# Performance work log

Hardware: AMD Instinct MI355X
Metric: run time of the kernel (lower is better)

Reference implementation:

```python
import jax, jax.numpy as jnp
import numpy as np

D = 2048          # hidden_size
H = 16            # num attention heads
HD = D // H       # head_dim = 128
DFF = 8192        # intermediate_size
DLCA = 4096       # d_lca = 2*hidden_size
EPS = 1e-6
LAM, TAU, DT, NSTEPS = 0.1, 0.1, 0.01, 10
ROPE_THETA = 10000.0


def rmsnorm(x, w):
    v = jnp.mean(x.astype(jnp.float32) ** 2, axis=-1, keepdims=True)
    return (x * jax.lax.rsqrt(v + EPS)).astype(x.dtype) * w


def rope_cos_sin(seq_len, dtype):
    inv_freq = 1.0 / (ROPE_THETA ** (jnp.arange(0, HD, 2, dtype=jnp.float32) / HD))
    t = jnp.arange(seq_len, dtype=jnp.float32)
    freqs = jnp.outer(t, inv_freq)              # [S, HD/2]
    emb = jnp.concatenate([freqs, freqs], -1)   # [S, HD]
    return jnp.cos(emb).astype(dtype), jnp.sin(emb).astype(dtype)


def rotate_half(x):
    x1, x2 = jnp.split(x, 2, axis=-1)
    return jnp.concatenate([-x2, x1], axis=-1)


def setup_inputs() -> dict:
    key = jax.random.key(0)
    ks = jax.random.split(key, 10)
    s = 0.02
    return {
        "hidden_states": jax.random.normal(ks[0], (2, 2048, D), jnp.float32),
        "w_ln_in": jnp.ones((D,), jnp.float32),
        "w_ln_lca": jnp.ones((D,), jnp.float32),
        "w_ln_post": jnp.ones((D,), jnp.float32),
        "Wq": jax.random.normal(ks[1], (D, D), jnp.float32) * s,
        "Wk": jax.random.normal(ks[2], (D, D), jnp.float32) * s,
        "Wv": jax.random.normal(ks[3], (D, D), jnp.float32) * s,
        "Wo": jax.random.normal(ks[4], (D, D), jnp.float32) * s,
        "W_lca": jax.random.normal(ks[5], (D, DLCA), jnp.float32) * s,
        "W_gate": jax.random.normal(ks[6], (D, DFF), jnp.float32) * s,
        "W_up": jax.random.normal(ks[7], (D, DFF), jnp.float32) * s,
        "W_down": jax.random.normal(ks[8], (DFF, D), jnp.float32) * s,
    }


def reference(hidden_states, w_ln_in, w_ln_lca, w_ln_post, Wq, Wk, Wv, Wo,
              W_lca, W_gate, W_up, W_down):
    B, S, _ = hidden_states.shape
    residual = hidden_states

    # --- causal self-attention with RoPE ---
    h = rmsnorm(hidden_states, w_ln_in)
    q = (h @ Wq).reshape(B, S, H, HD).transpose(0, 2, 1, 3)  # [B,H,S,HD]
    k = (h @ Wk).reshape(B, S, H, HD).transpose(0, 2, 1, 3)
    v = (h @ Wv).reshape(B, S, H, HD).transpose(0, 2, 1, 3)
    cos, sin = rope_cos_sin(S, h.dtype)
    q = q * cos + rotate_half(q) * sin
    k = k * cos + rotate_half(k) * sin
    scores = jnp.einsum('bhqd,bhkd->bhqk', q, k) / jnp.sqrt(jnp.asarray(HD, h.dtype))
    causal = jnp.tril(jnp.ones((S, S), bool))
    scores = jnp.where(causal, scores, jnp.finfo(scores.dtype).min)
    probs = jax.nn.softmax(scores, axis=-1)
    attn = jnp.einsum('bhqk,bhkd->bhqd', probs, v)
    attn = attn.transpose(0, 2, 1, 3).reshape(B, S, D) @ Wo
    h = residual + attn

    # --- LCA: project up, 10-step lateral-competition recurrence, project back ---
    hn = rmsnorm(h, w_ln_lca)
    xf = hn.reshape(-1, D)                       # [B*S, D]
    b = xf @ W_lca                               # [B*S, DLCA]
    G = W_lca.T @ W_lca                          # [DLCA, DLCA]
    G = G - jnp.diag(jnp.diag(G))                # zero diagonal (self-inhibition)
    u = jnp.zeros_like(b)
    for _ in range(NSTEPS):
        a = jax.nn.relu(u - LAM)
        u = u + DT * ((b - a @ G - u) / TAU)
    a = jax.nn.relu(u - LAM)
    h = (a @ W_lca.T).reshape(B, S, D)           # LCA REPLACES the residual stream

    # --- MLP (SwiGLU) with residual ---
    residual = h
    m = rmsnorm(h, w_ln_post)
    mlp = (jax.nn.silu(m @ W_gate) * (m @ W_up)) @ W_down
    return residual + mlp
```

## Files before the change

kernel.cpp:

```cpp
#include <hip/hip_runtime.h>
#include <hip/hip_fp8.h>

typedef short bf16x8 __attribute__((ext_vector_type(8)));
typedef float f32x4 __attribute__((ext_vector_type(4)));
typedef long long ll;

__device__ __forceinline__ unsigned short f2bf(float f) {
    union { float f; unsigned u; } v; v.f = f;
    unsigned u = v.u;
    unsigned r = (u + 0x7FFFu + ((u >> 16) & 1u)) >> 16;
    return (unsigned short)r;
}
__device__ __forceinline__ float bf2f(unsigned short h) {
    union { unsigned u; float f; } v; v.u = ((unsigned)h) << 16; return v.f;
}
__device__ __forceinline__ unsigned char f2fp8(float f) {
    __hip_fp8_e4m3 q(f);
    return (unsigned char)q.__x;
}

typedef const __attribute__((address_space(1))) void gas_void;
typedef __attribute__((address_space(3))) void las_void;
__device__ __forceinline__ void gll16(const void* g, void* l) {
    __builtin_amdgcn_global_load_lds((gas_void*)g, (las_void*)l, 16, 0, 0);
}

__global__ __launch_bounds__(256) void gemm_bf16(
    const unsigned short* __restrict__ A, ll lda, ll sAz,
    const unsigned short* __restrict__ B, ll ldb, ll sBz,
    void* __restrict__ C, ll ldc, ll sCz,
    int M, int N, int K,
    float alpha, int mode, int causal,
    const float* __restrict__ res)
{
    __shared__ unsigned short sA[2][4096];
    __shared__ unsigned short sB[2][4096];
    const int n0 = blockIdx.x * 128;
    const int m0 = blockIdx.y * 128;
    if (causal && n0 > m0) return;
    const int z = blockIdx.z;

    const unsigned short* Ab = A + (ll)z * sAz + (ll)m0 * lda;
    const unsigned short* Bb = B + (ll)z * sBz + (ll)n0 * ldb;

    const int t    = threadIdx.x;
    const int lane = t & 63;
    const int w    = t >> 6, wm = w >> 1, wn = w & 1;
    const int m16  = lane & 15, quad = lane >> 4;

    const int r0 = t >> 2, cs = t & 3;
    const int r1 = r0 + 64;
    const int c0 = cs ^ ((r0 >> 1) & 3);
    const int c1 = cs ^ ((r1 >> 1) & 3);
    const ll a_off0 = (ll)r0 * lda + c0 * 8;
    const ll a_off1 = (ll)r1 * lda + c1 * 8;
    const ll b_off0 = (ll)r0 * ldb + c0 * 8;
    const ll b_off1 = (ll)r1 * ldb + c1 * 8;
    const int dst = t * 8;

    int aoff[4], boff[4];
#pragma unroll
    for (int mi = 0; mi < 4; mi++) {
        int rr = wm * 64 + mi * 16 + m16;
        aoff[mi] = rr * 32 + ((quad ^ ((rr >> 1) & 3)) << 3);
    }
#pragma unroll
    for (int ni = 0; ni < 4; ni++) {
        int rr = wn * 64 + ni * 16 + m16;
        boff[ni] = rr * 32 + ((quad ^ ((rr >> 1) & 3)) << 3);
    }

    f32x4 acc[4][4];
#pragma unroll
    for (int i = 0; i < 4; i++)
#pragma unroll
        for (int j = 0; j < 4; j++) acc[i][j] = (f32x4){0.f, 0.f, 0.f, 0.f};

    gll16(Ab + a_off0, sA[0] + dst);
    gll16(Ab + a_off1, sA[0] + 2048 + dst);
    gll16(Bb + b_off0, sB[0] + dst);
    gll16(Bb + b_off1, sB[0] + 2048 + dst);
    __syncthreads();

    for (int kt = 0; kt < K; kt += 32) {
        const int cur = (kt >> 5) & 1;
        if (kt + 32 < K) {
            const int nxt = cur ^ 1;
            gll16(Ab + a_off0 + kt + 32, sA[nxt] + dst);
            gll16(Ab + a_off1 + kt + 32, sA[nxt] + 2048 + dst);
            gll16(Bb + b_off0 + kt + 32, sB[nxt] + dst);
            gll16(Bb + b_off1 + kt + 32, sB[nxt] + 2048 + dst);
        }
        bf16x8 af[4], bg[4];
#pragma unroll
        for (int mi = 0; mi < 4; mi++) af[mi] = *(const bf16x8*)(sA[cur] + aoff[mi]);
#pragma unroll
        for (int ni = 0; ni < 4; ni++) bg[ni] = *(const bf16x8*)(sB[cur] + boff[ni]);
#pragma unroll
        for (int mi = 0; mi < 4; mi++)
#pragma unroll
            for (int ni = 0; ni < 4; ni++)
                acc[mi][ni] = __builtin_amdgcn_mfma_f32_16x16x32_bf16(
                    af[mi], bg[ni], acc[mi][ni], 0, 0, 0);
        __syncthreads();
    }

    const ll czoff = (ll)z * sCz;
#pragma unroll
    for (int mi = 0; mi < 4; mi++) {
#pragma unroll
        for (int ni = 0; ni < 4; ni++) {
#pragma unroll
            for (int r = 0; r < 4; r++) {
                int row = m0 + wm * 64 + mi * 16 + quad * 4 + r;
                int col = n0 + wn * 64 + ni * 16 + m16;
                ll idx = czoff + (ll)row * ldc + col;
                float v = acc[mi][ni][r] * alpha;
                if (mode == 0) {
                    ((float*)C)[idx] = res ? (v + res[idx]) : v;
                } else if (mode == 1) {
                    ((unsigned short*)C)[idx] = f2bf(v);
                } else {
                    ((unsigned char*)C)[idx] = (row == col) ? (unsigned char)0 : f2fp8(v);
                }
            }
        }
    }
}

__global__ __launch_bounds__(256) void gemm_fp8(
    const unsigned char* __restrict__ A, ll lda,
    const unsigned char* __restrict__ B, ll ldb,
    int M, int N, int K, float alpha, int mode,
    unsigned short* __restrict__ uu, const unsigned short* __restrict__ cc,
    void* __restrict__ Out)
{
    __shared__ unsigned char sA[2][8192];
    __shared__ unsigned char sB[2][8192];
    const int n0 = blockIdx.x * 128;
    const int m0 = blockIdx.y * 128;

    const unsigned char* Ab = A + (ll)m0 * lda;
    const unsigned char* Bb = B + (ll)n0 * ldb;

    const int t    = threadIdx.x;
    const int lane = t & 63;
    const int w    = t >> 6, wm = w >> 1, wn = w & 1;
    const int m16  = lane & 15, quad = lane >> 4;

    const int r0 = t >> 2, cs = t & 3;
    const int r1 = r0 + 64;
    const int c0 = cs ^ ((r0 >> 1) & 3);
    const int c1 = cs ^ ((r1 >> 1) & 3);
    const ll a_off0 = (ll)r0 * lda + c0 * 16;
    const ll a_off1 = (ll)r1 * lda + c1 * 16;
    const ll b_off0 = (ll)r0 * ldb + c0 * 16;
    const ll b_off1 = (ll)r1 * ldb + c1 * 16;
    const int dst = t * 16;

    int aoff[4][2], boff[4][2];
#pragma unroll
    for (int mi = 0; mi < 4; mi++) {
        int rr = wm * 64 + mi * 16 + m16;
#pragma unroll
        for (int kh = 0; kh < 2; kh++) {
            int ch = kh * 2 + (quad >> 1);
            aoff[mi][kh] = rr * 64 + ((ch ^ ((rr >> 1) & 3)) << 4) + ((quad & 1) << 3);
        }
    }
#pragma unroll
    for (int ni = 0; ni < 4; ni++) {
        int rr = wn * 64 + ni * 16 + m16;
#pragma unroll
        for (int kh = 0; kh < 2; kh++) {
            int ch = kh * 2 + (quad >> 1);
            boff[ni][kh] = rr * 64 + ((ch ^ ((rr >> 1) & 3)) << 4) + ((quad & 1) << 3);
        }
    }

    f32x4 acc[4][4];
#pragma unroll
    for (int i = 0; i < 4; i++)
#pragma unroll
        for (int j = 0; j < 4; j++) acc[i][j] = (f32x4){0.f, 0.f, 0.f, 0.f};

    gll16(Ab + a_off0, sA[0] + dst);
    gll16(Ab + a_off1, sA[0] + 4096 + dst);
    gll16(Bb + b_off0, sB[0] + dst);
    gll16(Bb + b_off1, sB[0] + 4096 + dst);
    __syncthreads();

    for (int kt = 0; kt < K; kt += 64) {
        const int cur = (kt >> 6) & 1;
        if (kt + 64 < K) {
            const int nxt = cur ^ 1;
            gll16(Ab + a_off0 + kt + 64, sA[nxt] + dst);
            gll16(Ab + a_off1 + kt + 64, sA[nxt] + 4096 + dst);
            gll16(Bb + b_off0 + kt + 64, sB[nxt] + dst);
            gll16(Bb + b_off1 + kt + 64, sB[nxt] + 4096 + dst);
        }
#pragma unroll
        for (int kh = 0; kh < 2; kh++) {
            long long af[4], bg[4];
#pragma unroll
            for (int mi = 0; mi < 4; mi++)
                af[mi] = *(const long long*)(sA[cur] + aoff[mi][kh]);
#pragma unroll
            for (int ni = 0; ni < 4; ni++)
                bg[ni] = *(const long long*)(sB[cur] + boff[ni][kh]);
#pragma unroll
            for (int mi = 0; mi < 4; mi++)
#pragma unroll
                for (int ni = 0; ni < 4; ni++)
                    acc[mi][ni] = __builtin_amdgcn_mfma_f32_16x16x32_fp8_fp8(
                        af[mi], bg[ni], acc[mi][ni], 0, 0, 0);
        }
        __syncthreads();
    }

#pragma unroll
    for (int mi = 0; mi < 4; mi++) {
#pragma unroll
        for (int ni = 0; ni < 4; ni++) {
#pragma unroll
            for (int r = 0; r < 4; r++) {
                int row = m0 + wm * 64 + mi * 16 + quad * 4 + r;
                int col = n0 + wn * 64 + ni * 16 + m16;
                ll idx = (ll)row * N + col;
                float v = acc[mi][ni][r] * alpha;
                float un = 0.9f * bf2f(uu[idx]) + bf2f(cc[idx]) - v;
                uu[idx] = f2bf(un);
                float a = fmaxf(un - 0.1f, 0.0f);
                if (mode == 3) ((unsigned char*)Out)[idx] = f2fp8(a * 8.0f);
                else           ((unsigned short*)Out)[idx] = f2bf(a);
            }
        }
    }
}


__global__ void wtrans_k(const float* __restrict__ in, unsigned short* __restrict__ out,
                         int R, int C) {
    __shared__ float tile[32][33];
    ll bx = (ll)blockIdx.x * 32, by = (ll)blockIdx.y * 32;
    int tx = threadIdx.x & 31, ty = threadIdx.x >> 5;
#pragma unroll
    for (int i = ty; i < 32; i += 8) tile[i][tx] = in[(by + i) * C + bx + tx];
    __syncthreads();
#pragma unroll
    for (int i = ty; i < 32; i += 8) out[(bx + i) * R + by + tx] = f2bf(tile[tx][i]);
}

__global__ void conv4_k(const float* __restrict__ in, unsigned short* __restrict__ out, ll n) {
    ll i = ((ll)blockIdx.x * 256 + threadIdx.x) * 4;
    if (i >= n) return;
    float4 v = *(const float4*)(in + i);
    out[i] = f2bf(v.x); out[i + 1] = f2bf(v.y); out[i + 2] = f2bf(v.z); out[i + 3] = f2bf(v.w);
}

__global__ void rmsnorm_k(const float* __restrict__ in, const float* __restrict__ w,
                          unsigned short* __restrict__ out) {
    int row = blockIdx.x, t = threadIdx.x;
    const float* x = in + (ll)row * 2048;
    float v[8]; float s = 0.f;
#pragma unroll
    for (int i = 0; i < 8; i++) { v[i] = x[t + i * 256]; s += v[i] * v[i]; }
#pragma unroll
    for (int o = 32; o > 0; o >>= 1) s += __shfl_xor(s, o, 64);
    __shared__ float rs[4];
    if ((t & 63) == 0) rs[t >> 6] = s;
    __syncthreads();
    s = (rs[0] + rs[1] + rs[2] + rs[3]) * (1.0f / 2048.0f);
    float sc = rsqrtf(s + 1e-6f);
    unsigned short* o_ = out + (ll)row * 2048;
#pragma unroll
    for (int i = 0; i < 8; i++) o_[t + i * 256] = f2bf(v[i] * sc * w[t + i * 256]);
}

__global__ void rope_k(unsigned short* __restrict__ q, unsigned short* __restrict__ k) {
    int idx = blockIdx.x * 256 + threadIdx.x;
    int j = idx & 63;
    int h = (idx >> 6) & 15;
    int row = idx >> 10;
    int s = row & 2047;
    float f = __expf(-(float)j * 0.14391156831212783f);
    float ang = (float)s * f;
    float sn, cs;
    sincosf(ang, &sn, &cs);
    ll base = (ll)row * 2048 + h * 128 + j;
    float x1 = bf2f(q[base]), x2 = bf2f(q[base + 64]);
    q[base]      = f2bf(x1 * cs - x2 * sn);
    q[base + 64] = f2bf(x2 * cs + x1 * sn);
    x1 = bf2f(k[base]); x2 = bf2f(k[base + 64]);
    k[base]      = f2bf(x1 * cs - x2 * sn);
    k[base + 64] = f2bf(x2 * cs + x1 * sn);
}

__global__ void vtrans_k(const unsigned short* __restrict__ in, unsigned short* __restrict__ out) {
    __shared__ unsigned short tile[32][33];
    int z = blockIdx.z, b = z >> 4, h = z & 15;
    const unsigned short* ib = in + (ll)b * 4194304 + h * 128;
    unsigned short* ob = out + (ll)z * 262144;
    int bx = blockIdx.x * 32, by = blockIdx.y * 32;
    int tx = threadIdx.x & 31, ty = threadIdx.x >> 5;
#pragma unroll
    for (int i = ty; i < 32; i += 8) tile[i][tx] = ib[(ll)(by + i) * 2048 + bx + tx];
    __syncthreads();
#pragma unroll
    for (int i = ty; i < 32; i += 8) ob[(ll)(bx + i) * 2048 + by + tx] = tile[tx][i];
}

__global__ void softmax_k(unsigned short* __restrict__ sc) {
    int q = blockIdx.x, z = blockIdx.y, t = threadIdx.x;
    unsigned short* row = sc + (ll)z * 4194304 + (ll)q * 2048;
    float x[8]; float m = -1e30f;
#pragma unroll
    for (int i = 0; i < 8; i++) {
        int kk = t + i * 256;
        x[i] = (kk <= q) ? bf2f(row[kk]) : -1e30f;
        m = fmaxf(m, x[i]);
    }
#pragma unroll
    for (int o = 32; o > 0; o >>= 1) m = fmaxf(m, __shfl_xor(m, o, 64));
    __shared__ float rm[4];
    if ((t & 63) == 0) rm[t >> 6] = m;
    __syncthreads();
    m = fmaxf(fmaxf(rm[0], rm[1]), fmaxf(rm[2], rm[3]));
    float s = 0.f;
#pragma unroll
    for (int i = 0; i < 8; i++) {
        int kk = t + i * 256;
        float e = (kk <= q) ? __expf(x[i] - m) : 0.0f;
        x[i] = e; s += e;
    }
#pragma unroll
    for (int o = 32; o > 0; o >>= 1) s += __shfl_xor(s, o, 64);
    __shared__ float rsum[4];
    if ((t & 63) == 0) rsum[t >> 6] = s;
    __syncthreads();
    s = rsum[0] + rsum[1] + rsum[2] + rsum[3];
    float inv = 1.0f / s;
#pragma unroll
    for (int i = 0; i < 8; i++) row[t + i * 256] = f2bf(x[i] * inv);
}

__global__ void lca_init_k(const unsigned short* __restrict__ c, unsigned short* __restrict__ u,
                           unsigned char* __restrict__ a) {
    ll i = ((ll)blockIdx.x * 256 + threadIdx.x) * 4;
#pragma unroll
    for (int j = 0; j < 4; j++) {
        unsigned short cv = c[i + j];
        u[i + j] = cv;
        a[i + j] = f2fp8(fmaxf(bf2f(cv) - 0.1f, 0.f) * 8.0f);
    }
}

__global__ void swiglu_k(unsigned short* __restrict__ g, const unsigned short* __restrict__ u) {
    ll i = ((ll)blockIdx.x * 256 + threadIdx.x) * 4;
#pragma unroll
    for (int j = 0; j < 4; j++) {
        float x = bf2f(g[i + j]);
        float y = bf2f(u[i + j]);
        float sil = x / (1.0f + __expf(-x));
        g[i + j] = f2bf(sil * y);
    }
}

extern "C" void kernel_launch(void* const* d_in, const int* in_sizes, int n_in,
                              void* d_out, int out_size, void* d_ws, size_t ws_size,
                              hipStream_t stream) {
    (void)in_sizes; (void)n_in; (void)out_size; (void)ws_size;
    const float* X        = (const float*)d_in[0];
    const float* wln_in   = (const float*)d_in[1];
    const float* wln_lca  = (const float*)d_in[2];
    const float* wln_post = (const float*)d_in[3];
    const float* Wq   = (const float*)d_in[4];
    const float* Wk   = (const float*)d_in[5];
    const float* Wv   = (const float*)d_in[6];
    const float* Wo   = (const float*)d_in[7];
    const float* Wlca = (const float*)d_in[8];
    const float* Wg   = (const float*)d_in[9];
    const float* Wu   = (const float*)d_in[10];
    const float* Wd   = (const float*)d_in[11];
    float* out = (float*)d_out;

    char* ws = (char*)d_ws;
    unsigned short* WqT = (unsigned short*)(ws);
    unsigned short* WkT = WqT + 4194304;
    unsigned short* WvT = WqT + 2 * 4194304;
    unsigned short* WoT = WqT + 3 * 4194304;
    unsigned short* WgT = WqT;
    unsigned short* WlcaT = (unsigned short*)(ws + 33554432);
    unsigned short* Wlcab = WlcaT + 8388608;
    unsigned short* WuT   = WlcaT;
    unsigned short* h_bf = (unsigned short*)(ws + 67108864);
    char* pool = ws + 83886080;
    unsigned short* qb     = (unsigned short*)(pool);
    unsigned short* kb     = (unsigned short*)(pool + 16777216);
    unsigned short* vb     = (unsigned short*)(pool + 33554432);
    unsigned short* VT     = (unsigned short*)(pool + 50331648);
    unsigned short* attn   = (unsigned short*)(pool + 67108864);
    unsigned short* scores = (unsigned short*)(pool + 83886080);
    float* h1              = (float*)(pool + 150994944);
    unsigned short* cbuf   = (unsigned short*)(pool);
    unsigned short* ubuf   = (unsigned short*)(pool + 33554432);
    unsigned char* a8_0    = (unsigned char*)(pool + 67108864);
    unsigned char* a8_1    = (unsigned char*)(pool + 83886080);
    unsigned short* abf    = (unsigned short*)(pool + 100663296);
    unsigned char* Gf8     = (unsigned char*)(pool + 134217728);
    float* h2              = (float*)(pool + 150994944);
    unsigned short* gate   = (unsigned short*)(pool);
    unsigned short* up     = (unsigned short*)(pool + 67108864);
    unsigned short* WdT    = (unsigned short*)(pool + 201326592);

    dim3 blk(256);
    auto gemm = [&](const unsigned short* A, ll lda, ll sAz,
                    const unsigned short* Bt, ll ldb, ll sBz,
                    void* C, ll ldc, ll sCz,
                    int M, int N, int K, int Z,
                    float alpha, int mode, int causal, const float* res) {
        dim3 g(N / 128, M / 128, Z);
        gemm_bf16<<<g, blk, 0, stream>>>(A, lda, sAz, Bt, ldb, sBz, C, ldc, sCz,
                                         M, N, K, alpha, mode, causal, res);
    };

    wtrans_k<<<dim3(64, 64), blk, 0, stream>>>(Wq, WqT, 2048, 2048);
    wtrans_k<<<dim3(64, 64), blk, 0, stream>>>(Wk, WkT, 2048, 2048);
    wtrans_k<<<dim3(64, 64), blk, 0, stream>>>(Wv, WvT, 2048, 2048);
    wtrans_k<<<dim3(64, 64), blk, 0, stream>>>(Wo, WoT, 2048, 2048);
    wtrans_k<<<dim3(128, 64), blk, 0, stream>>>(Wlca, WlcaT, 2048, 4096);
    conv4_k<<<8192, blk, 0, stream>>>(Wlca, Wlcab, 8388608LL);

    rmsnorm_k<<<4096, blk, 0, stream>>>(X, wln_in, h_bf);
    gemm(h_bf, 2048, 0, WqT, 2048, 0, qb, 2048, 0, 4096, 2048, 2048, 1, 1.f, 1, 0, nullptr);
    gemm(h_bf, 2048, 0, WkT, 2048, 0, kb, 2048, 0, 4096, 2048, 2048, 1, 1.f, 1, 0, nullptr);
    gemm(h_bf, 2048, 0, WvT, 2048, 0, vb, 2048, 0, 4096, 2048, 2048, 1, 1.f, 1, 0, nullptr);
    rope_k<<<16384, blk, 0, stream>>>(qb, kb);
    vtrans_k<<<dim3(4, 64, 32), blk, 0, stream>>>(vb, VT);
    for (int c = 0; c < 4; c++) {
        int b = c >> 1, h0 = (c & 1) * 8;
        const unsigned short* qbase = qb + (ll)b * 4194304 + h0 * 128;
        const unsigned short* kbase = kb + (ll)b * 4194304 + h0 * 128;
        gemm(qbase, 2048, 128, kbase, 2048, 128, scores, 2048, 4194304LL,
             2048, 2048, 128, 8, 0.08838834764831845f, 1, 1, nullptr);
        softmax_k<<<dim3(2048, 8), blk, 0, stream>>>(scores);
        const unsigned short* vtb = VT + (ll)(b * 16 + h0) * 262144;
        unsigned short* ab = attn + (ll)b * 4194304 + h0 * 128;
        gemm(scores, 2048, 4194304LL, vtb, 2048, 262144LL, ab, 2048, 128,
             2048, 128, 2048, 8, 1.f, 1, 0, nullptr);
    }
    gemm(attn, 2048, 0, WoT, 2048, 0, h1, 2048, 0, 4096, 2048, 2048, 1, 1.f, 0, 0, X);

    rmsnorm_k<<<4096, blk, 0, stream>>>(h1, wln_lca, h_bf);
    gemm(WlcaT, 2048, 0, WlcaT, 2048, 0, Gf8, 4096, 0, 4096, 4096, 2048, 1, 16.f, 2, 0, nullptr);
    gemm(h_bf, 2048, 0, WlcaT, 2048, 0, cbuf, 4096, 0, 4096, 4096, 2048, 1, 0.1f, 1, 0, nullptr);
    lca_init_k<<<16384, blk, 0, stream>>>(cbuf, ubuf, a8_0);
    unsigned char* acur = a8_0; unsigned char* anext = a8_1;
    for (int i = 0; i < 9; i++) {
        int mode = (i < 8) ? 3 : 4;
        void* outp = (i < 8) ? (void*)anext : (void*)abf;
        gemm_fp8<<<dim3(32, 32), blk, 0, stream>>>(
            acur, 4096, Gf8, 4096, 4096, 4096, 4096,
            0.1f / 128.0f, mode, ubuf, cbuf, outp);
        unsigned char* tmp = acur; acur = anext; anext = tmp;
    }
    gemm(abf, 4096, 0, Wlcab, 4096, 0, h2, 2048, 0, 4096, 2048, 4096, 1, 1.f, 0, 0, nullptr);

    wtrans_k<<<dim3(256, 64), blk, 0, stream>>>(Wg, WgT, 2048, 8192);
    wtrans_k<<<dim3(256, 64), blk, 0, stream>>>(Wu, WuT, 2048, 8192);
    wtrans_k<<<dim3(64, 256), blk, 0, stream>>>(Wd, WdT, 8192, 2048);
    rmsnorm_k<<<4096, blk, 0, stream>>>(h2, wln_post, h_bf);
    gemm(h_bf, 2048, 0, WgT, 2048, 0, gate, 8192, 0, 4096, 8192, 2048, 1, 1.f, 1, 0, nullptr);
    gemm(h_bf, 2048, 0, WuT, 2048, 0, up, 8192, 0, 4096, 8192, 2048, 1, 1.f, 1, 0, nullptr);
    swiglu_k<<<32768, blk, 0, stream>>>(gate, up);
    gemm(gate, 8192, 0, WdT, 8192, 0, out, 2048, 0, 4096, 2048, 8192, 1, 1.f, 0, 0, h2);
}
```

Measured before the change: 3.324 ms.

## Add 256-tile pipelined bf16/fp8 GEMMs and fuse QKV and gate/up projections

Adds new 512-thread GEMM kernels: a 256x256 bf16 kernel, a 128x256 bf16 kernel with a triple-buffered LDS ring, and a 256x256 fp8 kernel for the LCA recurrence. All use XCD-aware workgroup remapping, interleaved LDS prefetch, and MFMA priority bumps. The Q/K/V projections become one GEMM into a fused [4096,6144] buffer, and gate/up become one GEMM into [4096,16384], so rope, vtrans, attention and swiglu now index the interleaved layouts. The larger tiles increase operand reuse and cut launch count, at the cost of more registers and LDS per block and fewer blocks on the smaller GEMMs. The fused QKV GEMM reads its weights from WqT with ldb 2048 across 6144 output columns, which assumes WqT, WkT and WvT sit contiguously in the workspace.

```diff
diff --git a/kernel.cpp b/kernel.cpp
--- a/kernel.cpp
+++ b/kernel.cpp
@@ -23,6 +23,445 @@
 typedef __attribute__((address_space(3))) void las_void;
 __device__ __forceinline__ void gll16(const void* g, void* l) {
     __builtin_amdgcn_global_load_lds((gas_void*)g, (las_void*)l, 16, 0, 0);
+}
+
+#define BAR __builtin_amdgcn_s_barrier()
+#define LGKM0 do { asm volatile("s_waitcnt lgkmcnt(0)" ::: "memory"); __builtin_amdgcn_sched_barrier(0); } while (0)
+#define VMC(n) asm volatile("s_waitcnt vmcnt(" #n ")" ::: "memory")
+
+__global__ __launch_bounds__(512, 2) void gemm256_k(
+    const unsigned short* __restrict__ A, ll lda,
+    const unsigned short* __restrict__ B, ll ldb,
+    void* __restrict__ C, ll ldc,
+    int K, float alpha, int mode, const float* __restrict__ res)
+{
+    __shared__ unsigned short sA[2][2][8192];
+    __shared__ unsigned short sB[2][2][8192];
+
+    const int nwg = gridDim.x * gridDim.y;
+    int id = blockIdx.y * gridDim.x + blockIdx.x;
+    { int q = nwg >> 3, r = nwg & 7, x = id & 7, bb = id >> 3;
+      id = (x < r ? x * (q + 1) : r * (q + 1) + (x - r) * q) + bb; }
+    const int n0 = (id % gridDim.x) * 256;
+    const int m0 = (id / gridDim.x) * 256;
+
+    const unsigned short* Ab = A + (ll)m0 * lda;
+    const unsigned short* Bb = B + (ll)n0 * ldb;
+
+    const int t = threadIdx.x;
+    const int lane = t & 63;
+    const int w = t >> 6, wm = w >> 2, wn = w & 3;
+    const int m16 = lane & 15, quad = lane >> 4;
+
+    const int tr = t >> 3;
+    const int tc8 = ((t & 7) ^ (tr & 7)) << 3;
+
+    const int pk0 = m16 * 64 + (((quad    ) ^ (m16 & 7)) << 3);
+    const int pk1 = m16 * 64 + (((4 + quad) ^ (m16 & 7)) << 3);
+
+    auto stA = [&](int tile, int h) {
+        char* d0 = (char*)&sA[tile & 1][h][0] + t * 16;
+        const unsigned short* s0 = Ab + (ll)(h * 128 + tr) * lda + tc8 + (ll)tile * 64;
+        gll16(s0, d0);
+        gll16(s0 + 64 * lda, d0 + 8192);
+    };
+    auto stB = [&](int tile, int h) {
+        char* d0 = (char*)&sB[tile & 1][h][0] + t * 16;
+        const unsigned short* s0 = Bb + (ll)(h * 128 + tr) * ldb + tc8 + (ll)tile * 64;
+        gll16(s0, d0);
+        gll16(s0 + 64 * ldb, d0 + 8192);
+    };
+    auto ldA = [&](int s, int g, bf16x8 (&af)[4][2]) {
+        const unsigned short* p0 = &sA[s][wm][g * 4096];
+#pragma unroll
+        for (int a2 = 0; a2 < 4; a2++) {
+            af[a2][0] = *(const bf16x8*)(p0 + a2 * 1024 + pk0);
+            af[a2][1] = *(const bf16x8*)(p0 + a2 * 1024 + pk1);
+        }
+    };
+    auto ldB = [&](int s, int g, bf16x8 (&bg)[2][2]) {
+        const unsigned short* p0 = &sB[s][wn >> 1][(wn & 1) * 4096 + g * 2048];
+#pragma unroll
+        for (int b2 = 0; b2 < 2; b2++) {
+            bg[b2][0] = *(const bf16x8*)(p0 + b2 * 1024 + pk0);
+            bg[b2][1] = *(const bf16x8*)(p0 + b2 * 1024 + pk1);
+        }
+    };
+
+    f32x4 acc[8][4];
+#pragma unroll
+    for (int i = 0; i < 8; i++)
+#pragma unroll
+        for (int j = 0; j < 4; j++) acc[i][j] = (f32x4){0.f, 0.f, 0.f, 0.f};
+
+    bf16x8 afA[4][2], afB[4][2], bgA[2][2], bgB[2][2];
+
+#define MM256(af, bg, gm, gn) do { \
+    __builtin_amdgcn_s_setprio(1); \
+    _Pragma("unroll") \
+    for (int a2 = 0; a2 < 4; a2++) \
+    _Pragma("unroll") \
+    for (int b2 = 0; b2 < 2; b2++) { \
+        acc[(gm)*4+a2][(gn)*2+b2] = __builtin_amdgcn_mfma_f32_16x16x32_bf16(af[a2][0], bg[b2][0], acc[(gm)*4+a2][(gn)*2+b2], 0, 0, 0); \
+        acc[(gm)*4+a2][(gn)*2+b2] = __builtin_amdgcn_mfma_f32_16x16x32_bf16(af[a2][1], bg[b2][1], acc[(gm)*4+a2][(gn)*2+b2], 0, 0, 0); \
+    } \
+    __builtin_amdgcn_s_setprio(0); \
+} while (0)
+
+    stB(0, 0); stB(0, 1); stA(0, 0); stA(0, 1); stB(1, 0); stB(1, 1);
+    VMC(4); BAR;
+
+#define ITER256(T, LAST) do { \
+     \
+    stA((T) + 1, 0); \
+    ldA(0, 0, afA); ldB(0, 0, bgA); \
+    BAR; LGKM0; \
+    MM256(afA, bgA, 0, 0); \
+    BAR; \
+     \
+    stA((T) + 1, 1); \
+    ldB(0, 1, bgB); \
+    BAR; LGKM0; \
+    MM256(afA, bgB, 0, 1); \
+    BAR; \
+     \
+    if (!(LAST)) stB((T) + 2, 0); \
+    ldA(0, 1, afB); \
+    BAR; LGKM0; \
+    MM256(afB, bgA, 1, 0); \
+    BAR; \
+     \
+    if (!(LAST)) stB((T) + 2, 1); \
+    MM256(afB, bgB, 1, 1); \
+    if (LAST) { VMC(0); } else { VMC(4); } \
+    BAR; \
+     \
+    if (!(LAST)) stA((T) + 2, 0); \
+    ldA(1, 0, afA); ldB(1, 0, bgA); \
+    BAR; LGKM0; \
+    MM256(afA, bgA, 0, 0); \
+    BAR; \
+     \
+    if (!(LAST)) stA((T) + 2, 1); \
+    ldB(1, 1, bgB); \
+    BAR; LGKM0; \
+    MM256(afA, bgB, 0, 1); \
+    BAR; \
+     \
+    if (!(LAST)) stB((T) + 3, 0); \
+    ldA(1, 1, afB); \
+    BAR; LGKM0; \
+    MM256(afB, bgA, 1, 0); \
+    BAR; \
+     \
+    if (!(LAST)) stB((T) + 3, 1); \
+    MM256(afB, bgB, 1, 1); \
+    if (!(LAST)) { VMC(4); BAR; } \
+} while (0)
+
+    const int nIter = K >> 7;
+    for (int i = 0; i < nIter - 1; ++i) ITER256(2 * i, false);
+    ITER256(2 * (nIter - 1), true);
+
+#pragma unroll
+    for (int mi = 0; mi < 8; mi++) {
+#pragma unroll
+        for (int ni = 0; ni < 4; ni++) {
+#pragma unroll
+            for (int r4 = 0; r4 < 4; r4++) {
+                int row = m0 + wm * 128 + mi * 16 + quad * 4 + r4;
+                int col = n0 + wn * 64 + ni * 16 + m16;
+                ll idx = (ll)row * ldc + col;
+                float v = acc[mi][ni][r4] * alpha;
+                if (mode == 0) ((float*)C)[idx] = res ? (v + res[idx]) : v;
+                else if (mode == 1) ((unsigned short*)C)[idx] = f2bf(v);
+                else ((unsigned char*)C)[idx] = (row == col) ? (unsigned char)0 : f2fp8(v);
+            }
+        }
+    }
+}
+
+__global__ __launch_bounds__(512, 2) void gemm128_k(
+    const unsigned short* __restrict__ A, ll lda,
+    const unsigned short* __restrict__ B, ll ldb,
+    void* __restrict__ C, ll ldc,
+    int K, float alpha, int mode, const float* __restrict__ res)
+{
+    __shared__ unsigned short sA[3][8192];
+    __shared__ unsigned short sB[3][2][8192];
+
+    const int nwg = gridDim.x * gridDim.y;
+    int id = blockIdx.y * gridDim.x + blockIdx.x;
+    { int q = nwg >> 3, r = nwg & 7, x = id & 7, bb = id >> 3;
+      id = (x < r ? x * (q + 1) : r * (q + 1) + (x - r) * q) + bb; }
+    const int n0 = (id % gridDim.x) * 256;
+    const int m0 = (id / gridDim.x) * 128;
+
+    const unsigned short* Ab = A + (ll)m0 * lda;
+    const unsigned short* Bb = B + (ll)n0 * ldb;
+
+    const int t = threadIdx.x;
+    const int lane = t & 63;
+    const int w = t >> 6, wm = w >> 2, wn = w & 3;
+    const int m16 = lane & 15, quad = lane >> 4;
+
+    const int tr = t >> 3;
+    const int tc8 = ((t & 7) ^ (tr & 7)) << 3;
+    const int pk0 = m16 * 64 + (((quad    ) ^ (m16 & 7)) << 3);
+    const int pk1 = m16 * 64 + (((4 + quad) ^ (m16 & 7)) << 3);
+
+    auto stA = [&](int tile, int s) {
+        char* d0 = (char*)&sA[s][0] + t * 16;
+        const unsigned short* s0 = Ab + (ll)tr * lda + tc8 + (ll)tile * 64;
+        gll16(s0, d0);
+        gll16(s0 + 64 * lda, d0 + 8192);
+    };
+    auto stB2 = [&](int tile, int s) {
+#pragma unroll
+        for (int h = 0; h < 2; h++) {
+            char* d0 = (char*)&sB[s][h][0] + t * 16;
+            const unsigned short* s0 = Bb + (ll)(h * 128 + tr) * ldb + tc8 + (ll)tile * 64;
+            gll16(s0, d0);
+            gll16(s0 + 64 * ldb, d0 + 8192);
+        }
+    };
+    auto ldA4 = [&](int s, bf16x8 (&af)[4][2]) {
+        const unsigned short* p0 = &sA[s][wm * 4096];
+#pragma unroll
+        for (int a2 = 0; a2 < 4; a2++) {
+            af[a2][0] = *(const bf16x8*)(p0 + a2 * 1024 + pk0);
+            af[a2][1] = *(const bf16x8*)(p0 + a2 * 1024 + pk1);
+        }
+    };
+    auto ldB2 = [&](int s, int g, bf16x8 (&bg)[2][2]) {
+        const unsigned short* p0 = &sB[s][wn >> 1][(wn & 1) * 4096 + g * 2048];
+#pragma unroll
+        for (int b2 = 0; b2 < 2; b2++) {
+            bg[b2][0] = *(const bf16x8*)(p0 + b2 * 1024 + pk0);
+            bg[b2][1] = *(const bf16x8*)(p0 + b2 * 1024 + pk1);
+        }
+    };
+
+    f32x4 acc[4][4];
+#pragma unroll
+    for (int i = 0; i < 4; i++)
+#pragma unroll
+        for (int j = 0; j < 4; j++) acc[i][j] = (f32x4){0.f, 0.f, 0.f, 0.f};
+
+    bf16x8 af[4][2], bgA[2][2], bgB[2][2];
+
+#define MM128(bg, gn) do { \
+    __builtin_amdgcn_s_setprio(1); \
+    _Pragma("unroll") \
+    for (int a2 = 0; a2 < 4; a2++) \
+    _Pragma("unroll") \
+    for (int b2 = 0; b2 < 2; b2++) { \
+        acc[a2][(gn)*2+b2] = __builtin_amdgcn_mfma_f32_16x16x32_bf16(af[a2][0], bg[b2][0], acc[a2][(gn)*2+b2], 0, 0, 0); \
+        acc[a2][(gn)*2+b2] = __builtin_amdgcn_mfma_f32_16x16x32_bf16(af[a2][1], bg[b2][1], acc[a2][(gn)*2+b2], 0, 0, 0); \
+    } \
+    __builtin_amdgcn_s_setprio(0); \
+} while (0)
+
+    stA(0, 0); stB2(0, 0); stA(1, 1); stB2(1, 1);
+    VMC(6); BAR;
+
+    const int nT = K >> 6;
+    int sl = 0;
+    for (int T = 0; T < nT - 2; ++T) {
+        const int s2 = (sl >= 1) ? sl - 1 : 2;
+        stA(T + 2, s2);
+        ldA4(sl, af); ldB2(sl, 0, bgA);
+        BAR; LGKM0;
+        MM128(bgA, 0);
+        BAR;
+        stB2(T + 2, s2);
+        ldB2(sl, 1, bgB);
+        BAR; LGKM0;
+        MM128(bgB, 1);
+        VMC(6);
+        BAR;
+        sl = (sl >= 2) ? 0 : sl + 1;
+    }
+    {
+        ldA4(sl, af); ldB2(sl, 0, bgA);
+        BAR; LGKM0;
+        MM128(bgA, 0);
+        BAR;
+        ldB2(sl, 1, bgB);
+        BAR; LGKM0;
+        MM128(bgB, 1);
+        VMC(0);
+        BAR;
+        sl = (sl >= 2) ? 0 : sl + 1;
+    }
+    {
+        ldA4(sl, af); ldB2(sl, 0, bgA);
+        LGKM0;
+        MM128(bgA, 0);
+        ldB2(sl, 1, bgB);
+        LGKM0;
+        MM128(bgB, 1);
+    }
+
+#pragma unroll
+    for (int mi = 0; mi < 4; mi++) {
+#pragma unroll
+        for (int ni = 0; ni < 4; ni++) {
+#pragma unroll
+            for (int r4 = 0; r4 < 4; r4++) {
+                int row = m0 + wm * 64 + mi * 16 + quad * 4 + r4;
+                int col = n0 + wn * 64 + ni * 16 + m16;
+                ll idx = (ll)row * ldc + col;
+                float v = acc[mi][ni][r4] * alpha;
+                if (mode == 0) ((float*)C)[idx] = res ? (v + res[idx]) : v;
+                else if (mode == 1) ((unsigned short*)C)[idx] = f2bf(v);
+                else ((unsigned char*)C)[idx] = (row == col) ? (unsigned char)0 : f2fp8(v);
+            }
+        }
+    }
+}
+
+__global__ __launch_bounds__(512, 2) void gemm256f8_k(
+    const unsigned char* __restrict__ A, ll lda,
+    const unsigned char* __restrict__ B, ll ldb,
+    int N, int K, float alpha, int mode,
+    unsigned short* __restrict__ uu, const unsigned short* __restrict__ cc,
+    void* __restrict__ Out)
+{
+    __shared__ unsigned char sA[2][2][8192];
+    __shared__ unsigned char sB[2][2][8192];
+
+    const int nwg = gridDim.x * gridDim.y;
+    int id = blockIdx.y * gridDim.x + blockIdx.x;
+    { int q = nwg >> 3, r = nwg & 7, x = id & 7, bb = id >> 3;
+      id = (x < r ? x * (q + 1) : r * (q + 1) + (x - r) * q) + bb; }
+    const int n0 = (id % gridDim.x) * 256;
+    const int m0 = (id / gridDim.x) * 256;
+
+    const unsigned char* Ab = A + (ll)m0 * lda;
+    const unsigned char* Bb = B + (ll)n0 * ldb;
+
+    const int t = threadIdx.x;
+    const int lane = t & 63;
+    const int w = t >> 6, wm = w >> 2, wn = w & 3;
+    const int m16 = lane & 15, quad = lane >> 4;
+
+    const int tr8 = t >> 2;
+    const int tc16 = (((t & 3) ^ ((t >> 3) & 3)) << 4);
+
+    const int pq0 = m16 * 64 + ((((quad >> 1))     ^ ((m16 >> 1) & 3)) << 4) + ((quad & 1) << 3);
+    const int pq1 = m16 * 64 + (((2 + (quad >> 1)) ^ ((m16 >> 1) & 3)) << 4) + ((quad & 1) << 3);
+
+    auto stA = [&](int tile, int h) {
+        gll16(Ab + (ll)(h * 128 + tr8) * lda + tc16 + (ll)tile * 64,
+              (char*)&sA[tile & 1][h][0] + t * 16);
+    };
+    auto stB = [&](int tile, int h) {
+        gll16(Bb + (ll)(h * 128 + tr8) * ldb + tc16 + (ll)tile * 64,
+              (char*)&sB[tile & 1][h][0] + t * 16);
+    };
+    auto ldA8 = [&](int s, int g, ll (&af)[4][2]) {
+        const unsigned char* p0 = &sA[s][wm][g * 4096];
+#pragma unroll
+        for (int a2 = 0; a2 < 4; a2++) {
+            af[a2][0] = *(const ll*)(p0 + a2 * 1024 + pq0);
+            af[a2][1] = *(const ll*)(p0 + a2 * 1024 + pq1);
+        }
+    };
+    auto ldB8 = [&](int s, int g, ll (&bg)[2][2]) {
+        const unsigned char* p0 = &sB[s][wn >> 1][(wn & 1) * 4096 + g * 2048];
+#pragma unroll
+        for (int b2 = 0; b2 < 2; b2++) {
+            bg[b2][0] = *(const ll*)(p0 + b2 * 1024 + pq0);
+            bg[b2][1] = *(const ll*)(p0 + b2 * 1024 + pq1);
+        }
+    };
+
+    f32x4 acc[8][4];
+#pragma unroll
+    for (int i = 0; i < 8; i++)
+#pragma unroll
+        for (int j = 0; j < 4; j++) acc[i][j] = (f32x4){0.f, 0.f, 0.f, 0.f};
+
+    ll afA[4][2], afB[4][2], bgA[2][2], bgB[2][2];
+
+#define MMF8(af, bg, gm, gn) do { \
+    __builtin_amdgcn_s_setprio(1); \
+    _Pragma("unroll") \
+    for (int a2 = 0; a2 < 4; a2++) \
+    _Pragma("unroll") \
+    for (int b2 = 0; b2 < 2; b2++) { \
+        acc[(gm)*4+a2][(gn)*2+b2] = __builtin_amdgcn_mfma_f32_16x16x32_fp8_fp8(af[a2][0], bg[b2][0], acc[(gm)*4+a2][(gn)*2+b2], 0, 0, 0); \
+        acc[(gm)*4+a2][(gn)*2+b2] = __builtin_amdgcn_mfma_f32_16x16x32_fp8_fp8(af[a2][1], bg[b2][1], acc[(gm)*4+a2][(gn)*2+b2], 0, 0, 0); \
+    } \
+    __builtin_amdgcn_s_setprio(0); \
+} while (0)
+
+    stB(0, 0); stB(0, 1); stA(0, 0); stA(0, 1); stB(1, 0); stB(1, 1);
+    VMC(2); BAR;
+
+#define ITERF8(T, LAST) do { \
+    stA((T) + 1, 0); \
+    ldA8(0, 0, afA); ldB8(0, 0, bgA); \
+    BAR; LGKM0; \
+    MMF8(afA, bgA, 0, 0); \
+    BAR; \
+    stA((T) + 1, 1); \
+    ldB8(0, 1, bgB); \
+    BAR; LGKM0; \
+    MMF8(afA, bgB, 0, 1); \
+    BAR; \
+    if (!(LAST)) stB((T) + 2, 0); \
+    ldA8(0, 1, afB); \
+    BAR; LGKM0; \
+    MMF8(afB, bgA, 1, 0); \
+    BAR; \
+    if (!(LAST)) stB((T) + 2, 1); \
+    MMF8(afB, bgB, 1, 1); \
+    if (LAST) { VMC(0); } else { VMC(2); } \
+    BAR; \
+    if (!(LAST)) stA((T) + 2, 0); \
+    ldA8(1, 0, afA); ldB8(1, 0, bgA); \
+    BAR; LGKM0; \
+    MMF8(afA, bgA, 0, 0); \
+    BAR; \
+    if (!(LAST)) stA((T) + 2, 1); \
+    ldB8(1, 1, bgB); \
+    BAR; LGKM0; \
+    MMF8(afA, bgB, 0, 1); \
+    BAR; \
+    if (!(LAST)) stB((T) + 3, 0); \
+    ldA8(1, 1, afB); \
+    BAR; LGKM0; \
+    MMF8(afB, bgA, 1, 0); \
+    BAR; \
+    if (!(LAST)) stB((T) + 3, 1); \
+    MMF8(afB, bgB, 1, 1); \
+    if (!(LAST)) { VMC(2); BAR; } \
+} while (0)
+
+    const int nIter = K >> 7;
+    for (int i = 0; i < nIter - 1; ++i) ITERF8(2 * i, false);
+    ITERF8(2 * (nIter - 1), true);
+
+#pragma unroll
+    for (int mi = 0; mi < 8; mi++) {
+#pragma unroll
+        for (int ni = 0; ni < 4; ni++) {
+#pragma unroll
+            for (int r = 0; r < 4; r++) {
+                int row = m0 + wm * 128 + mi * 16 + quad * 4 + r;
+                int col = n0 + wn * 64 + ni * 16 + m16;
+                ll idx = (ll)row * N + col;
+                float v = acc[mi][ni][r] * alpha;
+                float un = 0.9f * bf2f(uu[idx]) + bf2f(cc[idx]) - v;
+                uu[idx] = f2bf(un);
+                float a = fmaxf(un - 0.1f, 0.0f);
+                if (mode == 3) ((unsigned char*)Out)[idx] = f2fp8(a * 8.0f);
+                else           ((unsigned short*)Out)[idx] = f2bf(a);
+            }
+        }
+    }
 }
 
 __global__ __launch_bounds__(256) void gemm_bf16(
@@ -128,116 +567,6 @@
     }
 }
 
-__global__ __launch_bounds__(256) void gemm_fp8(
-    const unsigned char* __restrict__ A, ll lda,
-    const unsigned char* __restrict__ B, ll ldb,
-    int M, int N, int K, float alpha, int mode,
-    unsigned short* __restrict__ uu, const unsigned short* __restrict__ cc,
-    void* __restrict__ Out)
-{
-    __shared__ unsigned char sA[2][8192];
-    __shared__ unsigned char sB[2][8192];
-    const int n0 = blockIdx.x * 128;
-    const int m0 = blockIdx.y * 128;
-
-    const unsigned char* Ab = A + (ll)m0 * lda;
-    const unsigned char* Bb = B + (ll)n0 * ldb;
-
-    const int t    = threadIdx.x;
-    const int lane = t & 63;
-    const int w    = t >> 6, wm = w >> 1, wn = w & 1;
-    const int m16  = lane & 15, quad = lane >> 4;
-
-    const int r0 = t >> 2, cs = t & 3;
-    const int r1 = r0 + 64;
-    const int c0 = cs ^ ((r0 >> 1) & 3);
-    const int c1 = cs ^ ((r1 >> 1) & 3);
-    const ll a_off0 = (ll)r0 * lda + c0 * 16;
-    const ll a_off1 = (ll)r1 * lda + c1 * 16;
-    const ll b_off0 = (ll)r0 * ldb + c0 * 16;
-    const ll b_off1 = (ll)r1 * ldb + c1 * 16;
-    const int dst = t * 16;
-
-    int aoff[4][2], boff[4][2];
-#pragma unroll
-    for (int mi = 0; mi < 4; mi++) {
-        int rr = wm * 64 + mi * 16 + m16;
-#pragma unroll
-        for (int kh = 0; kh < 2; kh++) {
-            int ch = kh * 2 + (quad >> 1);
-            aoff[mi][kh] = rr * 64 + ((ch ^ ((rr >> 1) & 3)) << 4) + ((quad & 1) << 3);
-        }
-    }
-#pragma unroll
-    for (int ni = 0; ni < 4; ni++) {
-        int rr = wn * 64 + ni * 16 + m16;
-#pragma unroll
-        for (int kh = 0; kh < 2; kh++) {
-            int ch = kh * 2 + (quad >> 1);
-            boff[ni][kh] = rr * 64 + ((ch ^ ((rr >> 1) & 3)) << 4) + ((quad & 1) << 3);
-        }
-    }
-
-    f32x4 acc[4][4];
-#pragma unroll
-    for (int i = 0; i < 4; i++)
-#pragma unroll
-        for (int j = 0; j < 4; j++) acc[i][j] = (f32x4){0.f, 0.f, 0.f, 0.f};
-
-    gll16(Ab + a_off0, sA[0] + dst);
-    gll16(Ab + a_off1, sA[0] + 4096 + dst);
-    gll16(Bb + b_off0, sB[0] + dst);
-    gll16(Bb + b_off1, sB[0] + 4096 + dst);
-    __syncthreads();
-
-    for (int kt = 0; kt < K; kt += 64) {
-        const int cur = (kt >> 6) & 1;
-        if (kt + 64 < K) {
-            const int nxt = cur ^ 1;
-            gll16(Ab + a_off0 + kt + 64, sA[nxt] + dst);
-            gll16(Ab + a_off1 + kt + 64, sA[nxt] + 4096 + dst);
-            gll16(Bb + b_off0 + kt + 64, sB[nxt] + dst);
-            gll16(Bb + b_off1 + kt + 64, sB[nxt] + 4096 + dst);
-        }
-#pragma unroll
-        for (int kh = 0; kh < 2; kh++) {
-            long long af[4], bg[4];
-#pragma unroll
-            for (int mi = 0; mi < 4; mi++)
-                af[mi] = *(const long long*)(sA[cur] + aoff[mi][kh]);
-#pragma unroll
-            for (int ni = 0; ni < 4; ni++)
-                bg[ni] = *(const long long*)(sB[cur] + boff[ni][kh]);
-#pragma unroll
-            for (int mi = 0; mi < 4; mi++)
-#pragma unroll
-                for (int ni = 0; ni < 4; ni++)
-                    acc[mi][ni] = __builtin_amdgcn_mfma_f32_16x16x32_fp8_fp8(
-                        af[mi], bg[ni], acc[mi][ni], 0, 0, 0);
-        }
-        __syncthreads();
-    }
-
-#pragma unroll
-    for (int mi = 0; mi < 4; mi++) {
-#pragma unroll
-        for (int ni = 0; ni < 4; ni++) {
-#pragma unroll
-            for (int r = 0; r < 4; r++) {
-                int row = m0 + wm * 64 + mi * 16 + quad * 4 + r;
-                int col = n0 + wn * 64 + ni * 16 + m16;
-                ll idx = (ll)row * N + col;
-                float v = acc[mi][ni][r] * alpha;
-                float un = 0.9f * bf2f(uu[idx]) + bf2f(cc[idx]) - v;
-                uu[idx] = f2bf(un);
-                float a = fmaxf(un - 0.1f, 0.0f);
-                if (mode == 3) ((unsigned char*)Out)[idx] = f2fp8(a * 8.0f);
-                else           ((unsigned short*)Out)[idx] = f2bf(a);
-            }
-        }
-    }
-}
-
 
 __global__ void wtrans_k(const float* __restrict__ in, unsigned short* __restrict__ out,
                          int R, int C) {
@@ -277,7 +606,7 @@
     for (int i = 0; i < 8; i++) o_[t + i * 256] = f2bf(v[i] * sc * w[t + i * 256]);
 }
 
-__global__ void rope_k(unsigned short* __restrict__ q, unsigned short* __restrict__ k) {
+__global__ void rope_k(unsigned short* __restrict__ qkv) {
     int idx = blockIdx.x * 256 + threadIdx.x;
     int j = idx & 63;
     int h = (idx >> 6) & 15;
@@ -287,24 +616,24 @@
     float ang = (float)s * f;
     float sn, cs;
     sincosf(ang, &sn, &cs);
-    ll base = (ll)row * 2048 + h * 128 + j;
-    float x1 = bf2f(q[base]), x2 = bf2f(q[base + 64]);
-    q[base]      = f2bf(x1 * cs - x2 * sn);
-    q[base + 64] = f2bf(x2 * cs + x1 * sn);
-    x1 = bf2f(k[base]); x2 = bf2f(k[base + 64]);
-    k[base]      = f2bf(x1 * cs - x2 * sn);
-    k[base + 64] = f2bf(x2 * cs + x1 * sn);
-}
-
-__global__ void vtrans_k(const unsigned short* __restrict__ in, unsigned short* __restrict__ out) {
+    ll base = (ll)row * 6144 + h * 128 + j;
+    float x1 = bf2f(qkv[base]), x2 = bf2f(qkv[base + 64]);
+    qkv[base]      = f2bf(x1 * cs - x2 * sn);
+    qkv[base + 64] = f2bf(x2 * cs + x1 * sn);
+    x1 = bf2f(qkv[base + 2048]); x2 = bf2f(qkv[base + 2112]);
+    qkv[base + 2048] = f2bf(x1 * cs - x2 * sn);
+    qkv[base + 2112] = f2bf(x2 * cs + x1 * sn);
+}
+
+__global__ void vtrans_k(const unsigned short* __restrict__ qkv, unsigned short* __restrict__ out) {
     __shared__ unsigned short tile[32][33];
     int z = blockIdx.z, b = z >> 4, h = z & 15;
-    const unsigned short* ib = in + (ll)b * 4194304 + h * 128;
+    const unsigned short* ib = qkv + (ll)b * 2048 * 6144 + 4096 + h * 128;
     unsigned short* ob = out + (ll)z * 262144;
     int bx = blockIdx.x * 32, by = blockIdx.y * 32;
     int tx = threadIdx.x & 31, ty = threadIdx.x >> 5;
 #pragma unroll
-    for (int i = ty; i < 32; i += 8) tile[i][tx] = ib[(ll)(by + i) * 2048 + bx + tx];
+    for (int i = ty; i < 32; i += 8) tile[i][tx] = ib[(ll)(by + i) * 6144 + bx + tx];
     __syncthreads();
 #pragma unroll
     for (int i = ty; i < 32; i += 8) ob[(ll)(bx + i) * 2048 + by + tx] = tile[tx][i];
@@ -355,14 +684,16 @@
     }
 }
 
-__global__ void swiglu_k(unsigned short* __restrict__ g, const unsigned short* __restrict__ u) {
+__global__ void swiglu_k(unsigned short* __restrict__ gu) {
     ll i = ((ll)blockIdx.x * 256 + threadIdx.x) * 4;
+    ll row = i >> 13, col = i & 8191;
+    unsigned short* g = gu + row * 16384 + col;
+    const unsigned short* u = g + 8192;
 #pragma unroll
     for (int j = 0; j < 4; j++) {
-        float x = bf2f(g[i + j]);
-        float y = bf2f(u[i + j]);
-        float sil = x / (1.0f + __expf(-x));
-        g[i + j] = f2bf(sil * y);
+        float x = bf2f(g[j]);
+        float y = bf2f(u[j]);
+        g[j] = f2bf(x / (1.0f + __expf(-x)) * y);
     }
 }
 
@@ -395,9 +726,7 @@
     unsigned short* WuT   = WlcaT;
     unsigned short* h_bf = (unsigned short*)(ws + 67108864);
     char* pool = ws + 83886080;
-    unsigned short* qb     = (unsigned short*)(pool);
-    unsigned short* kb     = (unsigned short*)(pool + 16777216);
-    unsigned short* vb     = (unsigned short*)(pool + 33554432);
+    unsigned short* qkv    = (unsigned short*)(pool);
     unsigned short* VT     = (unsigned short*)(pool + 50331648);
     unsigned short* attn   = (unsigned short*)(pool + 67108864);
     unsigned short* scores = (unsigned short*)(pool + 83886080);
@@ -409,8 +738,7 @@
     unsigned short* abf    = (unsigned short*)(pool + 100663296);
     unsigned char* Gf8     = (unsigned char*)(pool + 134217728);
     float* h2              = (float*)(pool + 150994944);
-    unsigned short* gate   = (unsigned short*)(pool);
-    unsigned short* up     = (unsigned short*)(pool + 67108864);
+    unsigned short* gu     = (unsigned short*)(pool);
     unsigned short* WdT    = (unsigned short*)(pool + 201326592);
 
     dim3 blk(256);
@@ -423,6 +751,18 @@
         gemm_bf16<<<g, blk, 0, stream>>>(A, lda, sAz, Bt, ldb, sBz, C, ldc, sCz,
                                          M, N, K, alpha, mode, causal, res);
     };
+    auto g256 = [&](const unsigned short* A, ll lda, const unsigned short* Bt, ll ldb,
+                    void* C, ll ldc, int M, int N, int K, float alpha, int mode,
+                    const float* res) {
+        dim3 g(N / 256, M / 256);
+        gemm256_k<<<g, dim3(512), 0, stream>>>(A, lda, Bt, ldb, C, ldc, K, alpha, mode, res);
+    };
+    auto g128 = [&](const unsigned short* A, ll lda, const unsigned short* Bt, ll ldb,
+                    void* C, ll ldc, int M, int N, int K, float alpha, int mode,
+                    const float* res) {
+        dim3 g(N / 256, M / 128);
+        gemm128_k<<<g, dim3(512), 0, stream>>>(A, lda, Bt, ldb, C, ldc, K, alpha, mode, res);
+    };
 
     wtrans_k<<<dim3(64, 64), blk, 0, stream>>>(Wq, WqT, 2048, 2048);
     wtrans_k<<<dim3(64, 64), blk, 0, stream>>>(Wk, WkT, 2048, 2048);
@@ -432,16 +772,14 @@
     conv4_k<<<8192, blk, 0, stream>>>(Wlca, Wlcab, 8388608LL);
 
     rmsnorm_k<<<4096, blk, 0, stream>>>(X, wln_in, h_bf);
-    gemm(h_bf, 2048, 0, WqT, 2048, 0, qb, 2048, 0, 4096, 2048, 2048, 1, 1.f, 1, 0, nullptr);
-    gemm(h_bf, 2048, 0, WkT, 2048, 0, kb, 2048, 0, 4096, 2048, 2048, 1, 1.f, 1, 0, nullptr);
-    gemm(h_bf, 2048, 0, WvT, 2048, 0, vb, 2048, 0, 4096, 2048, 2048, 1, 1.f, 1, 0, nullptr);
-    rope_k<<<16384, blk, 0, stream>>>(qb, kb);
-    vtrans_k<<<dim3(4, 64, 32), blk, 0, stream>>>(vb, VT);
+    g256(h_bf, 2048, WqT, 2048, qkv, 6144, 4096, 6144, 2048, 1.f, 1, nullptr);
+    rope_k<<<16384, blk, 0, stream>>>(qkv);
+    vtrans_k<<<dim3(4, 64, 32), blk, 0, stream>>>(qkv, VT);
     for (int c = 0; c < 4; c++) {
         int b = c >> 1, h0 = (c & 1) * 8;
-        const unsigned short* qbase = qb + (ll)b * 4194304 + h0 * 128;
-        const unsigned short* kbase = kb + (ll)b * 4194304 + h0 * 128;
-        gemm(qbase, 2048, 128, kbase, 2048, 128, scores, 2048, 4194304LL,
+        const unsigned short* qbase = qkv + (ll)b * 2048 * 6144 + h0 * 128;
+        const unsigned short* kbase = qbase + 2048;
+        gemm(qbase, 6144, 128, kbase, 6144, 128, scores, 2048, 4194304LL,
              2048, 2048, 128, 8, 0.08838834764831845f, 1, 1, nullptr);
         softmax_k<<<dim3(2048, 8), blk, 0, stream>>>(scores);
         const unsigned short* vtb = VT + (ll)(b * 16 + h0) * 262144;
@@ -449,29 +787,28 @@
         gemm(scores, 2048, 4194304LL, vtb, 2048, 262144LL, ab, 2048, 128,
              2048, 128, 2048, 8, 1.f, 1, 0, nullptr);
     }
-    gemm(attn, 2048, 0, WoT, 2048, 0, h1, 2048, 0, 4096, 2048, 2048, 1, 1.f, 0, 0, X);
+    g128(attn, 2048, WoT, 2048, h1, 2048, 4096, 2048, 2048, 1.f, 0, X);
 
     rmsnorm_k<<<4096, blk, 0, stream>>>(h1, wln_lca, h_bf);
-    gemm(WlcaT, 2048, 0, WlcaT, 2048, 0, Gf8, 4096, 0, 4096, 4096, 2048, 1, 16.f, 2, 0, nullptr);
-    gemm(h_bf, 2048, 0, WlcaT, 2048, 0, cbuf, 4096, 0, 4096, 4096, 2048, 1, 0.1f, 1, 0, nullptr);
+    g256(WlcaT, 2048, WlcaT, 2048, Gf8, 4096, 4096, 4096, 2048, 16.f, 2, nullptr);
+    g256(h_bf, 2048, WlcaT, 2048, cbuf, 4096, 4096, 4096, 2048, 0.1f, 1, nullptr);
     lca_init_k<<<16384, blk, 0, stream>>>(cbuf, ubuf, a8_0);
     unsigned char* acur = a8_0; unsigned char* anext = a8_1;
     for (int i = 0; i < 9; i++) {
         int mode = (i < 8) ? 3 : 4;
         void* outp = (i < 8) ? (void*)anext : (void*)abf;
-        gemm_fp8<<<dim3(32, 32), blk, 0, stream>>>(
-            acur, 4096, Gf8, 4096, 4096, 4096, 4096,
+        gemm256f8_k<<<dim3(16, 16), dim3(512), 0, stream>>>(
+            acur, 4096, Gf8, 4096, 4096, 4096,
             0.1f / 128.0f, mode, ubuf, cbuf, outp);
         unsigned char* tmp = acur; acur = anext; anext = tmp;
     }
-    gemm(abf, 4096, 0, Wlcab, 4096, 0, h2, 2048, 0, 4096, 2048, 4096, 1, 1.f, 0, 0, nullptr);
+    g128(abf, 4096, Wlcab, 4096, h2, 2048, 4096, 2048, 4096, 1.f, 0, nullptr);
 
     wtrans_k<<<dim3(256, 64), blk, 0, stream>>>(Wg, WgT, 2048, 8192);
     wtrans_k<<<dim3(256, 64), blk, 0, stream>>>(Wu, WuT, 2048, 8192);
     wtrans_k<<<dim3(64, 256), blk, 0, stream>>>(Wd, WdT, 8192, 2048);
     rmsnorm_k<<<4096, blk, 0, stream>>>(h2, wln_post, h_bf);
-    gemm(h_bf, 2048, 0, WgT, 2048, 0, gate, 8192, 0, 4096, 8192, 2048, 1, 1.f, 1, 0, nullptr);
-    gemm(h_bf, 2048, 0, WuT, 2048, 0, up, 8192, 0, 4096, 8192, 2048, 1, 1.f, 1, 0, nullptr);
-    swiglu_k<<<32768, blk, 0, stream>>>(gate, up);
-    gemm(gate, 8192, 0, WdT, 8192, 0, out, 2048, 0, 4096, 2048, 8192, 1, 1.f, 0, 0, h2);
-}
+    g256(h_bf, 2048, WgT, 2048, gu, 16384, 4096, 16384, 2048, 1.f, 1, nullptr);
+    swiglu_k<<<32768, blk, 0, stream>>>(gu);
+    g128(gu, 16384, WdT, 8192, out, 2048, 4096, 2048, 8192, 1.f, 0, h2);
+}
```

Measured after the change: 3.286 ms. About the same (-1.2%).
